# Kernel tuning notes

Hardware: AMD Instinct MI355X
Metric: run time of the kernel (lower is better)

The kernel has to match this reference:

```python
import jax, jax.numpy as jnp
import numpy as np

N_ENT = 50000
N_REL = 500
N_DIM = 256
K = 4            # num_blocks; n_arity = 3 -> arch has K**3 = 64 entries
B = 1024


def setup_inputs() -> dict:
    key = jax.random.key(0)
    k0, k1, k2, k3 = jax.random.split(key, 4)
    facts = jax.random.randint(k0, (B, 3), 0, N_REL)          # head, tail, rela (all < n_rel <= n_ent)
    arch = jax.random.randint(k1, (K ** 3,), 0, 3)            # selects op in {0, 1, -1}
    ent_w = jax.random.normal(k2, (N_ENT, N_DIM), dtype=jnp.float32) * 0.05  # xavier-ish scale
    rel_w = jax.random.normal(k3, (N_REL, N_DIM), dtype=jnp.float32) * 0.05
    return {
        "facts": facts,
        "arch": arch,
        "ent_w": ent_w,
        "rel_w": rel_w,
        "bne_gamma": jnp.ones((N_DIM,), jnp.float32),
        "bne_beta": jnp.zeros((N_DIM,), jnp.float32),
        "bnr_gamma": jnp.ones((N_DIM,), jnp.float32),
        "bnr_beta": jnp.zeros((N_DIM,), jnp.float32),
    }


def _bn(x, gamma, beta, eps=1e-5):
    # BatchNorm1d in training mode: biased batch statistics over the batch dim.
    m = jnp.mean(x, axis=0)
    v = jnp.var(x, axis=0)
    return (x - m) * jax.lax.rsqrt(v + eps) * gamma + beta


def _bce(p, y):
    # torch F.binary_cross_entropy clamps log terms at -100
    logp = jnp.maximum(jnp.log(p), -100.0)
    log1mp = jnp.maximum(jnp.log1p(-p), -100.0)
    return -jnp.mean(y * logp + (1.0 - y) * log1mp)


def reference(facts, arch, ent_w, rel_w, bne_gamma, bne_beta, bnr_gamma, bnr_beta):
    L = N_DIM // K
    h, t, r = facts[:, 0], facts[:, 1], facts[:, 2]
    # separate BN calls for head / tail batches, as in the torch code (dropout is eval-mode identity)
    he = _bn(ent_w[h], bne_gamma, bne_beta).reshape(-1, K, L)   # [B, K, L]
    te = _bn(ent_w[t], bne_gamma, bne_beta).reshape(-1, K, L)
    re = _bn(rel_w[r], bnr_gamma, bnr_beta).reshape(-1, K, L)
    # alpha[i,j,k] = ops[op_idx[i*K*K + j*K + k]] in {0, 1, -1}
    alpha = jnp.asarray([0.0, 1.0, -1.0], dtype=ent_w.dtype)[arch].reshape(K, K, K)
    # fused extend + inner_vec + inner_alpha_bi + sum-over-blocks:
    # last_idx=2 (head side, rela x tail): vec[b,k,l] = sum_{i,j} alpha[i,j,k] r[b,i,l] t[b,j,l]
    head_vec = jnp.einsum('ijk,bil,bjl->bkl', alpha, re, te).reshape(-1, N_DIM)
    # last_idx=1 (tail side, rela x head): vec[b,k,l] = sum_{i,j} alpha[i,k,j] r[b,i,l] h[b,j,l]
    tail_vec = jnp.einsum('ikj,bil,bjl->bkl', alpha, re, he).reshape(-1, N_DIM)
    head_p = jax.nn.softmax(head_vec @ ent_w.T, axis=1)         # [B, N_ENT]
    tail_p = jax.nn.softmax(tail_vec @ ent_w.T, axis=1)
    head_label = jax.nn.one_hot(h, N_ENT, dtype=head_p.dtype)
    tail_label = jax.nn.one_hot(t, N_ENT, dtype=tail_p.dtype)
    return _bce(head_p, head_label) + _bce(tail_p, tail_label)
```

## Files before the change

kernel.cpp:

```cpp
#include <hip/hip_runtime.h>

#define N_ENT   50000
#define N_ENT_P 50176
#define NDIM    256
#define BATCH   1024
#define MROWS   2048
#define BM      128
#define BN      256
#define NTILES  196
#define NSTRIP  16
#define SHIFT   30.0f

typedef __attribute__((ext_vector_type(8))) short short8;
typedef __attribute__((ext_vector_type(4))) float f32x4;

__device__ __forceinline__ unsigned short f2bf(float f) {
  unsigned int u = __float_as_uint(f);
  u += 0x7fffu + ((u >> 16) & 1u);
  return (unsigned short)(u >> 16);
}

__device__ __forceinline__ void async16(const void* g, void* lds) {
  __builtin_amdgcn_global_load_lds(
      (const __attribute__((address_space(1))) unsigned int*)g,
      (__attribute__((address_space(3))) unsigned int*)lds,
      16, 0, 0);
}

__global__ void k_convert(const float* __restrict__ ent_w,
                          unsigned short* __restrict__ Wb) {
  int t = blockIdx.x * 256 + threadIdx.x;
  int row = t >> 6, c4 = (t & 63) << 2;
  ushort4 v;
  if (row < N_ENT) {
    float4 f = *(const float4*)(ent_w + row * NDIM + c4);
    v.x = f2bf(f.x); v.y = f2bf(f.y); v.z = f2bf(f.z); v.w = f2bf(f.w);
  } else {
    v.x = v.y = v.z = v.w = 0;
  }
  *(ushort4*)(Wb + row * NDIM + c4) = v;
}

__global__ void k_stats(const int* __restrict__ facts,
                        const float* __restrict__ ent_w,
                        const float* __restrict__ rel_w,
                        float* __restrict__ stats) {
  int seg = blockIdx.y;
  int d = threadIdx.x;
  const float* tab = (seg == 2) ? rel_w : ent_w;
  int r0 = blockIdx.x * 16;
  int idxs[16];
#pragma unroll
  for (int i = 0; i < 16; ++i) idxs[i] = facts[(r0 + i) * 3 + seg];
  float s = 0.f, s2 = 0.f;
#pragma unroll
  for (int i = 0; i < 16; ++i) {
    float v = tab[idxs[i] * NDIM + d];
    s += v; s2 += v * v;
  }
  atomicAdd(&stats[(seg * 2 + 0) * NDIM + d], s);
  atomicAdd(&stats[(seg * 2 + 1) * NDIM + d], s2);
}

__global__ void k_vectors(const int* __restrict__ facts, const int* __restrict__ arch,
                          const float* __restrict__ ent_w, const float* __restrict__ rel_w,
                          const float* __restrict__ bne_g, const float* __restrict__ bne_b,
                          const float* __restrict__ bnr_g, const float* __restrict__ bnr_b,
                          const float* __restrict__ stats,
                          unsigned short* __restrict__ HVb, float* __restrict__ zlab) {
  __shared__ float sh_he[256], sh_te[256], sh_re[256], sh_alpha[64], sh_red[16];
  int b = blockIdx.x, d = threadIdx.x;
  int h = facts[b * 3 + 0], t = facts[b * 3 + 1], r = facts[b * 3 + 2];
  const float inv = 1.0f / (float)BATCH;
  float mh = stats[0 * 256 + d] * inv, vh = stats[1 * 256 + d] * inv - mh * mh;
  float mt = stats[2 * 256 + d] * inv, vt = stats[3 * 256 + d] * inv - mt * mt;
  float mr = stats[4 * 256 + d] * inv, vr = stats[5 * 256 + d] * inv - mr * mr;
  float sch = rsqrtf(vh + 1e-5f) * bne_g[d], shh = bne_b[d] - mh * sch;
  float sct = rsqrtf(vt + 1e-5f) * bne_g[d], sht = bne_b[d] - mt * sct;
  float scr = rsqrtf(vr + 1e-5f) * bnr_g[d], shr = bnr_b[d] - mr * scr;
  sh_he[d] = ent_w[h * NDIM + d] * sch + shh;
  sh_te[d] = ent_w[t * NDIM + d] * sct + sht;
  sh_re[d] = rel_w[r * NDIM + d] * scr + shr;
  if (d < 64) {
    int a = arch[d];
    sh_alpha[d] = (a == 0) ? 0.f : ((a == 1) ? 1.f : -1.f);
  }
  __syncthreads();
  int k = d >> 6, l = d & 63;
  float hv = 0.f, tv = 0.f;
#pragma unroll
  for (int i = 0; i < 4; ++i) {
    float re_i = sh_re[i * 64 + l];
#pragma unroll
    for (int j = 0; j < 4; ++j) {
      hv += sh_alpha[i * 16 + j * 4 + k] * re_i * sh_te[j * 64 + l];
      tv += sh_alpha[i * 16 + k * 4 + j] * re_i * sh_he[j * 64 + l];
    }
  }
  HVb[b * NDIM + d] = f2bf(hv);
  HVb[(BATCH + b) * NDIM + d] = f2bf(tv);
  float ph = hv * ent_w[h * NDIM + d];
  float pt = tv * ent_w[t * NDIM + d];
  for (int m = 1; m < 64; m <<= 1) { ph += __shfl_xor(ph, m); pt += __shfl_xor(pt, m); }
  int wid = d >> 6;
  if ((d & 63) == 0) { sh_red[wid] = ph; sh_red[8 + wid] = pt; }
  __syncthreads();
  if (d == 0) {
    zlab[b] = sh_red[0] + sh_red[1] + sh_red[2] + sh_red[3];
    zlab[BATCH + b] = sh_red[8] + sh_red[9] + sh_red[10] + sh_red[11];
  }
}

__global__ void __launch_bounds__(512, 2)
k_gemm(const unsigned short* __restrict__ HVb, const unsigned short* __restrict__ Wb,
       float* __restrict__ m1, float* __restrict__ m2) {
  __shared__ __align__(16) unsigned short As[4 * BM * 64];
  __shared__ __align__(16) unsigned short Bs[4 * BN * 32];
  const int tid = threadIdx.x;
  const int lane = tid & 63, wid = tid >> 6;
  const int L = blockIdx.x;
  const int xcd = L & 7, rr = L >> 3;
  const int strip = xcd * 2 + (rr >> 4);
  const int bm = (rr & 15) * BM;
  const int wm = (wid >> 2) * 64, wn = (wid & 3) * 64;
  const int q = lane >> 4, ln = lane & 15;

  const int ntmine = NTILES / NSTRIP + (strip < (NTILES % NSTRIP) ? 1 : 0);
  const int njobs = ntmine * 8;

#pragma unroll
  for (int c = 0; c < 4; ++c)
#pragma unroll
    for (int i = 0; i < 2; ++i) {
      int G = (wid * 2 + i) * 64 + lane;
      int row = G >> 3, slot = G & 7;
      int kg = slot ^ (row & 7);
      async16(HVb + (bm + row) * NDIM + c * 64 + kg * 8,
              (char*)As + c * 16384 + (wid * 2 + i) * 1024);
    }

  auto stageB = [&](int j2) {
    int jj = (j2 < njobs) ? j2 : 0;
    int nt = strip + (jj >> 3) * NSTRIP;
    int kc = (jj & 7) * 32;
    int buf = j2 & 3;
#pragma unroll
    for (int i = 0; i < 2; ++i) {
      int G = (wid * 2 + i) * 64 + lane;
      int row = G >> 2, slot = G & 3;
      int kg = slot ^ ((row >> 1) & 3);
      async16(Wb + (nt * BN + row) * NDIM + kc + kg * 8,
              (char*)Bs + buf * 16384 + (wid * 2 + i) * 1024);
    }
  };
  stageB(0); stageB(1); stageB(2);

  float ps1[4][4] = {}, ps2[4][4] = {};
  int j = 0;
  for (int ti = 0; ti < ntmine; ++ti) {
    f32x4 acc[4][4] = {};
#pragma unroll
    for (int c = 0; c < 8; ++c, ++j) {
      asm volatile("s_waitcnt vmcnt(4)" ::: "memory");
      __builtin_amdgcn_s_barrier();
      asm volatile("" ::: "memory");
      stageB(j + 3);
      const char* Ac = (const char*)As + (c >> 1) * 16384;
      const char* Bc = (const char*)Bs + (c & 3) * 16384;
      const int kga = ((c & 1) << 2) + q;
      short8 a[4], bb[4];
#pragma unroll
      for (int mi = 0; mi < 4; ++mi) {
        int row = wm + mi * 16 + ln;
        a[mi] = *(const short8*)(Ac + row * 128 + ((kga ^ (row & 7)) << 4));
      }
#pragma unroll
      for (int ni = 0; ni < 4; ++ni) {
        int row = wn + ni * 16 + ln;
        bb[ni] = *(const short8*)(Bc + row * 64 + ((q ^ ((row >> 1) & 3)) << 4));
      }
#pragma unroll
      for (int mi = 0; mi < 4; ++mi)
#pragma unroll
        for (int ni = 0; ni < 4; ++ni)
          acc[mi][ni] = __builtin_amdgcn_mfma_f32_16x16x32_bf16(a[mi], bb[ni], acc[mi][ni], 0, 0, 0);
    }
#pragma unroll
    for (int mi = 0; mi < 4; ++mi)
#pragma unroll
      for (int reg = 0; reg < 4; ++reg) {
        float s1 = 0.f, s2 = 0.f;
#pragma unroll
        for (int ni = 0; ni < 4; ++ni) {
          float e1 = __expf(acc[mi][ni][reg] - SHIFT);
          s1 += e1; s2 += e1 * e1;
        }
        ps1[mi][reg] += s1;
        ps2[mi][reg] += s2;
      }
  }
  asm volatile("s_waitcnt vmcnt(0)" ::: "memory");

#pragma unroll
  for (int mi = 0; mi < 4; ++mi)
#pragma unroll
    for (int reg = 0; reg < 4; ++reg) {
      float s1 = ps1[mi][reg], s2 = ps2[mi][reg];
      for (int m = 1; m < 16; m <<= 1) { s1 += __shfl_xor(s1, m); s2 += __shfl_xor(s2, m); }
      if (ln == 0) {
        int grow = bm + wm + mi * 16 + q * 4 + reg;
        atomicAdd(&m1[grow], s1);
        atomicAdd(&m2[grow], s2);
      }
    }
}

__global__ void k_finalize(const float* __restrict__ m1, const float* __restrict__ m2,
                           const float* __restrict__ zlab, float* __restrict__ out) {
  __shared__ float red[16];
  int tid = threadIdx.x;
  float local = 0.f;
  for (int r = tid; r < MROWS; r += 1024) {
    float M1 = m1[r];
    float lse = SHIFT + logf(M1);
    float zl = zlab[r];
    float lp = fmaxf(zl - lse, -100.f);
    float pl = __expf(zl - lse);
    float l1m = fmaxf(log1pf(-pl), -100.f);
    float iM1 = 1.f / M1;
    float r2 = m2[r] * iM1 * iM1;
    float series = -(1.f + 0.5f * r2);
    local += lp - l1m + series;
  }
  for (int m = 1; m < 64; m <<= 1) local += __shfl_xor(local, m);
  if ((tid & 63) == 0) red[tid >> 6] = local;
  __syncthreads();
  if (tid == 0) {
    float s = 0.f;
    for (int i = 0; i < 16; ++i) s += red[i];
    out[0] = -s / ((float)BATCH * (float)N_ENT);
  }
}

extern "C" void kernel_launch(void* const* d_in, const int* in_sizes, int n_in,
                              void* d_out, int out_size, void* d_ws, size_t ws_size,
                              hipStream_t stream) {
  const int* facts = (const int*)d_in[0];
  const int* arch = (const int*)d_in[1];
  const float* ent_w = (const float*)d_in[2];
  const float* rel_w = (const float*)d_in[3];
  const float* bne_g = (const float*)d_in[4];
  const float* bne_b = (const float*)d_in[5];
  const float* bnr_g = (const float*)d_in[6];
  const float* bnr_b = (const float*)d_in[7];
  char* ws = (char*)d_ws;
  float* stats = (float*)ws;
  float* m1 = (float*)(ws + 6144);
  float* m2 = (float*)(ws + 14336);
  float* zlab = (float*)(ws + 22528);
  unsigned short* HVb = (unsigned short*)(ws + 30720);
  unsigned short* Wb = (unsigned short*)(ws + 30720 + 1048576);

  hipMemsetAsync(ws, 0, 22528, stream);
  k_convert<<<dim3((N_ENT_P * 64) / 256), dim3(256), 0, stream>>>(ent_w, Wb);
  k_stats<<<dim3(64, 3), dim3(256), 0, stream>>>(facts, ent_w, rel_w, stats);
  k_vectors<<<dim3(BATCH), dim3(256), 0, stream>>>(facts, arch, ent_w, rel_w,
                                                   bne_g, bne_b, bnr_g, bnr_b,
                                                   stats, HVb, zlab);
  k_gemm<<<dim3(256), dim3(512), 0, stream>>>(HVb, Wb, m1, m2);
  k_finalize<<<dim3(1), dim3(1024), 0, stream>>>(m1, m2, zlab, (float*)d_out);
}
```

Before: 176.6 us.

## Keep A operand in registers, drop A LDS tile, flush row sums per tile

The GEMM kernel now loads each wave's full 64x256 slice of the activation (A) matrix straight from global memory into registers once, instead of staging it through LDS and re-reading it every k-step. This removes the A LDS buffer and its per-step LDS reads, and precomputes the B LDS offsets. It also raises wave priority around the MFMA block. To free the partial-sum registers, the exp sums are now reduced and atomically added to global memory after every N tile rather than once at the end. The trade-offs are much higher VGPR pressure under the 512x2 launch bound, with a risk of spills, many more global atomics, and extra vector-memory operations that interact with the vmcnt-based pipelining waits.

```diff
diff --git a/kernel.cpp b/kernel.cpp
--- a/kernel.cpp
+++ b/kernel.cpp
@@ -114,7 +114,6 @@
 __global__ void __launch_bounds__(512, 2)
 k_gemm(const unsigned short* __restrict__ HVb, const unsigned short* __restrict__ Wb,
        float* __restrict__ m1, float* __restrict__ m2) {
-  __shared__ __align__(16) unsigned short As[4 * BM * 64];
   __shared__ __align__(16) unsigned short Bs[4 * BN * 32];
   const int tid = threadIdx.x;
   const int lane = tid & 63, wid = tid >> 6;
@@ -128,62 +127,58 @@
   const int ntmine = NTILES / NSTRIP + (strip < (NTILES % NSTRIP) ? 1 : 0);
   const int njobs = ntmine * 8;
 
-#pragma unroll
-  for (int c = 0; c < 4; ++c)
-#pragma unroll
-    for (int i = 0; i < 2; ++i) {
-      int G = (wid * 2 + i) * 64 + lane;
-      int row = G >> 3, slot = G & 7;
-      int kg = slot ^ (row & 7);
-      async16(HVb + (bm + row) * NDIM + c * 64 + kg * 8,
-              (char*)As + c * 16384 + (wid * 2 + i) * 1024);
-    }
-
-  auto stageB = [&](int j2) {
+  short8 a[4][8];
+#pragma unroll
+  for (int mi = 0; mi < 4; ++mi)
+#pragma unroll
+    for (int c = 0; c < 8; ++c)
+      a[mi][c] = *(const short8*)(HVb + (bm + wm + mi * 16 + ln) * NDIM + c * 32 + q * 8);
+
+  int boff[4];
+#pragma unroll
+  for (int ni = 0; ni < 4; ++ni) {
+    int row = wn + ni * 16 + ln;
+    boff[ni] = row * 64 + ((q ^ ((row >> 1) & 3)) << 4);
+  }
+
+  auto stageB = [&](int j2, int buf) {
     int jj = (j2 < njobs) ? j2 : 0;
     int nt = strip + (jj >> 3) * NSTRIP;
     int kc = (jj & 7) * 32;
-    int buf = j2 & 3;
+    const unsigned short* gbase = Wb + nt * (BN * NDIM) + kc;
 #pragma unroll
     for (int i = 0; i < 2; ++i) {
       int G = (wid * 2 + i) * 64 + lane;
       int row = G >> 2, slot = G & 3;
       int kg = slot ^ ((row >> 1) & 3);
-      async16(Wb + (nt * BN + row) * NDIM + kc + kg * 8,
+      async16(gbase + row * NDIM + kg * 8,
               (char*)Bs + buf * 16384 + (wid * 2 + i) * 1024);
     }
   };
-  stageB(0); stageB(1); stageB(2);
-
-  float ps1[4][4] = {}, ps2[4][4] = {};
+  stageB(0, 0); stageB(1, 1); stageB(2, 2);
+
   int j = 0;
   for (int ti = 0; ti < ntmine; ++ti) {
     f32x4 acc[4][4] = {};
 #pragma unroll
-    for (int c = 0; c < 8; ++c, ++j) {
+    for (int c = 0; c < 8; ++c) {
       asm volatile("s_waitcnt vmcnt(4)" ::: "memory");
       __builtin_amdgcn_s_barrier();
       asm volatile("" ::: "memory");
-      stageB(j + 3);
-      const char* Ac = (const char*)As + (c >> 1) * 16384;
+      stageB(j + 3, (c + 3) & 3);
       const char* Bc = (const char*)Bs + (c & 3) * 16384;
-      const int kga = ((c & 1) << 2) + q;
-      short8 a[4], bb[4];
-#pragma unroll
-      for (int mi = 0; mi < 4; ++mi) {
-        int row = wm + mi * 16 + ln;
-        a[mi] = *(const short8*)(Ac + row * 128 + ((kga ^ (row & 7)) << 4));
-      }
-#pragma unroll
-      for (int ni = 0; ni < 4; ++ni) {
-        int row = wn + ni * 16 + ln;
-        bb[ni] = *(const short8*)(Bc + row * 64 + ((q ^ ((row >> 1) & 3)) << 4));
-      }
+      short8 bb[4];
+#pragma unroll
+      for (int ni = 0; ni < 4; ++ni)
+        bb[ni] = *(const short8*)(Bc + boff[ni]);
+      __builtin_amdgcn_s_setprio(1);
 #pragma unroll
       for (int mi = 0; mi < 4; ++mi)
 #pragma unroll
         for (int ni = 0; ni < 4; ++ni)
-          acc[mi][ni] = __builtin_amdgcn_mfma_f32_16x16x32_bf16(a[mi], bb[ni], acc[mi][ni], 0, 0, 0);
+          acc[mi][ni] = __builtin_amdgcn_mfma_f32_16x16x32_bf16(a[mi][c], bb[ni], acc[mi][ni], 0, 0, 0);
+      __builtin_amdgcn_s_setprio(0);
+      ++j;
     }
 #pragma unroll
     for (int mi = 0; mi < 4; ++mi)
@@ -195,24 +190,15 @@
           float e1 = __expf(acc[mi][ni][reg] - SHIFT);
           s1 += e1; s2 += e1 * e1;
         }
-        ps1[mi][reg] += s1;
-        ps2[mi][reg] += s2;
+        for (int m = 1; m < 16; m <<= 1) { s1 += __shfl_xor(s1, m); s2 += __shfl_xor(s2, m); }
+        if (ln == 0) {
+          int grow = bm + wm + mi * 16 + q * 4 + reg;
+          atomicAdd(&m1[grow], s1);
+          atomicAdd(&m2[grow], s2);
+        }
       }
   }
   asm volatile("s_waitcnt vmcnt(0)" ::: "memory");
-
-#pragma unroll
-  for (int mi = 0; mi < 4; ++mi)
-#pragma unroll
-    for (int reg = 0; reg < 4; ++reg) {
-      float s1 = ps1[mi][reg], s2 = ps2[mi][reg];
-      for (int m = 1; m < 16; m <<= 1) { s1 += __shfl_xor(s1, m); s2 += __shfl_xor(s2, m); }
-      if (ln == 0) {
-        int grow = bm + wm + mi * 16 + q * 4 + reg;
-        atomicAdd(&m1[grow], s1);
-        atomicAdd(&m2[grow], s2);
-      }
-    }
 }
 
 __global__ void k_finalize(const float* __restrict__ m1, const float* __restrict__ m2,
```

Result: slower. 226.7 us (+28.4%).

## Software-pipeline LDS fragment reads with MFMA via double-buffered registers

Applied to the files above, without the earlier changes.

Restructures the GEMM inner loop so LDS reads for the next k-chunk are issued while MFMAs for the current chunk run, using two register fragment sets and sched_barrier to keep the ordering. Precomputes the swizzled LDS and global offsets outside the loop and raises wave priority around the MFMA block. The aim is to hide LDS latency and cut per-iteration address arithmetic. In exchange it uses more VGPRs and makes the barrier and buffer-index logic more fragile, with staging now four chunks ahead.

```diff
diff --git a/kernel.cpp b/kernel.cpp
--- a/kernel.cpp
+++ b/kernel.cpp
@@ -139,52 +139,84 @@
               (char*)As + c * 16384 + (wid * 2 + i) * 1024);
     }
 
-  auto stageB = [&](int j2) {
+  int aoffq[4], boff[4];
+#pragma unroll
+  for (int mi = 0; mi < 4; ++mi) {
+    int row = wm + mi * 16 + ln;
+    aoffq[mi] = row * 128 + ((q ^ (row & 7)) << 4);
+  }
+#pragma unroll
+  for (int ni = 0; ni < 4; ++ni) {
+    int row = wn + ni * 16 + ln;
+    boff[ni] = row * 64 + ((q ^ ((row >> 1) & 3)) << 4);
+  }
+
+  int ssoff[2], sdoff[2];
+#pragma unroll
+  for (int i = 0; i < 2; ++i) {
+    int G = (wid * 2 + i) * 64 + lane;
+    int row = G >> 2, slot = G & 3;
+    int kg = slot ^ ((row >> 1) & 3);
+    ssoff[i] = row * NDIM + kg * 8;
+    sdoff[i] = (wid * 2 + i) * 1024;
+  }
+  auto stageB = [&](int j2, int buf) {
     int jj = (j2 < njobs) ? j2 : 0;
     int nt = strip + (jj >> 3) * NSTRIP;
-    int kc = (jj & 7) * 32;
-    int buf = j2 & 3;
-#pragma unroll
-    for (int i = 0; i < 2; ++i) {
-      int G = (wid * 2 + i) * 64 + lane;
-      int row = G >> 2, slot = G & 3;
-      int kg = slot ^ ((row >> 1) & 3);
-      async16(Wb + (nt * BN + row) * NDIM + kc + kg * 8,
-              (char*)Bs + buf * 16384 + (wid * 2 + i) * 1024);
-    }
+    const unsigned short* gbase = Wb + nt * (BN * NDIM) + (jj & 7) * 32;
+#pragma unroll
+    for (int i = 0; i < 2; ++i)
+      async16(gbase + ssoff[i], (char*)Bs + buf * 16384 + sdoff[i]);
   };
-  stageB(0); stageB(1); stageB(2);
-
+  stageB(0, 0); stageB(1, 1); stageB(2, 2);
+
+  short8 fa0[4], fb0[4], fa1[4], fb1[4];
   float ps1[4][4] = {}, ps2[4][4] = {};
-  int j = 0;
+
+#define RD(CN, FA, FB)                                                        \
+  {                                                                           \
+    const char* Ac = (const char*)As + ((((CN)) & 7) >> 1) * 16384;           \
+    const char* Bc = (const char*)Bs + (((CN)) & 3) * 16384;                  \
+    const int axor = (((CN)) & 1) << 6;                                       \
+    _Pragma("unroll") for (int mi = 0; mi < 4; ++mi)                          \
+        FA[mi] = *(const short8*)(Ac + (aoffq[mi] ^ axor));                   \
+    _Pragma("unroll") for (int ni = 0; ni < 4; ++ni)                          \
+        FB[ni] = *(const short8*)(Bc + boff[ni]);                             \
+  }
+#define MM(FA, FB)                                                            \
+  {                                                                           \
+    __builtin_amdgcn_s_setprio(1);                                            \
+    _Pragma("unroll") for (int mi = 0; mi < 4; ++mi)                          \
+        _Pragma("unroll") for (int ni = 0; ni < 4; ++ni)                      \
+            acc[mi][ni] = __builtin_amdgcn_mfma_f32_16x16x32_bf16(            \
+                FA[mi], FB[ni], acc[mi][ni], 0, 0, 0);                        \
+    __builtin_amdgcn_s_setprio(0);                                            \
+  }
+#define PH(C, FAR, FBR, FAU, FBU)                                             \
+  asm volatile("s_waitcnt vmcnt(4)" ::: "memory");                            \
+  __builtin_amdgcn_s_barrier();                                               \
+  RD((C) + 1, FAR, FBR);                                                      \
+  stageB(ti * 8 + (C) + 4, ((C) + 4) & 3);                                    \
+  __builtin_amdgcn_sched_barrier(0);                                          \
+  MM(FAU, FBU);                                                               \
+  asm volatile("s_waitcnt lgkmcnt(0)" ::: "memory");
+
+  asm volatile("s_waitcnt vmcnt(4)" ::: "memory");
+  __builtin_amdgcn_s_barrier();
+  RD(0, fa0, fb0);
+  stageB(3, 3);
+  asm volatile("s_waitcnt lgkmcnt(0)" ::: "memory");
+
   for (int ti = 0; ti < ntmine; ++ti) {
     f32x4 acc[4][4] = {};
-#pragma unroll
-    for (int c = 0; c < 8; ++c, ++j) {
-      asm volatile("s_waitcnt vmcnt(4)" ::: "memory");
-      __builtin_amdgcn_s_barrier();
-      asm volatile("" ::: "memory");
-      stageB(j + 3);
-      const char* Ac = (const char*)As + (c >> 1) * 16384;
-      const char* Bc = (const char*)Bs + (c & 3) * 16384;
-      const int kga = ((c & 1) << 2) + q;
-      short8 a[4], bb[4];
-#pragma unroll
-      for (int mi = 0; mi < 4; ++mi) {
-        int row = wm + mi * 16 + ln;
-        a[mi] = *(const short8*)(Ac + row * 128 + ((kga ^ (row & 7)) << 4));
-      }
-#pragma unroll
-      for (int ni = 0; ni < 4; ++ni) {
-        int row = wn + ni * 16 + ln;
-        bb[ni] = *(const short8*)(Bc + row * 64 + ((q ^ ((row >> 1) & 3)) << 4));
-      }
-#pragma unroll
-      for (int mi = 0; mi < 4; ++mi)
-#pragma unroll
-        for (int ni = 0; ni < 4; ++ni)
-          acc[mi][ni] = __builtin_amdgcn_mfma_f32_16x16x32_bf16(a[mi], bb[ni], acc[mi][ni], 0, 0, 0);
-    }
+    PH(0, fa1, fb1, fa0, fb0)
+    PH(1, fa0, fb0, fa1, fb1)
+    PH(2, fa1, fb1, fa0, fb0)
+    PH(3, fa0, fb0, fa1, fb1)
+    PH(4, fa1, fb1, fa0, fb0)
+    PH(5, fa0, fb0, fa1, fb1)
+    PH(6, fa1, fb1, fa0, fb0)
+    PH(7, fa0, fb0, fa1, fb1)
 #pragma unroll
     for (int mi = 0; mi < 4; ++mi)
 #pragma unroll
@@ -199,6 +231,9 @@
         ps2[mi][reg] += s2;
       }
   }
+#undef PH
+#undef MM
+#undef RD
   asm volatile("s_waitcnt vmcnt(0)" ::: "memory");
 
 #pragma unroll
```

New measurement: 175.7 us. About the same (-0.5%).
